# Kernel optimization log

Hardware: AMD Instinct MI355X
Metric: run time of the kernel (lower is better)

The kernel has to match this reference:

```python
import jax, jax.numpy as jnp
import numpy as np
import math

B, L, HD, H = 4, 1024, 512, 8
D = HD // H  # 64 per-head dim


def setup_inputs() -> dict:
    key = jax.random.key(0)
    ks = jax.random.split(key, 9)
    query = jax.random.normal(ks[0], (B, L, HD), jnp.float32)
    key_ = jax.random.normal(ks[1], (B, L, HD), jnp.float32)
    value = jax.random.normal(ks[2], (B, L, HD), jnp.float32)
    kernel = jax.random.normal(ks[3], (B * H, L, L), jnp.float32) * 0.1
    # sparse-ish boolean mask; low density so no row is fully masked
    attn_mask = jax.random.bernoulli(ks[4], 0.05, (B * H, L, L))
    in_proj_weight = jax.random.normal(ks[5], (3 * HD, HD), jnp.float32) * 0.02
    in_proj_bias = jnp.zeros((3 * HD,), jnp.float32)
    out_w = jax.random.normal(ks[6], (HD, HD), jnp.float32) * 0.02
    out_b = jnp.zeros((HD,), jnp.float32)
    return dict(query=query, key_=key_, value=value, attn_mask=attn_mask,
                key_padding_mask=0, kernel=kernel,
                in_proj_weight=in_proj_weight, in_proj_bias=in_proj_bias,
                out_w=out_w, out_b=out_b)


def _split_heads(x):
    # [B, L, HD] -> [B*H, L, D]
    b, l, _ = x.shape
    return x.reshape(b, l, H, D).transpose(0, 2, 1, 3).reshape(b * H, l, D)


def _merge_heads(x):
    # [B*H, L, D] -> [B, L, HD]
    bh, l, d = x.shape
    b = bh // H
    return x.reshape(b, H, l, d).transpose(0, 2, 1, 3).reshape(b, l, H * d)


def reference(query, key_, value, attn_mask, key_padding_mask, kernel,
              in_proj_weight, in_proj_bias, out_w, out_b):
    # key_padding_mask is falsy (None-equivalent) -> attn_mask unchanged
    wq, wk, wv = in_proj_weight[:HD], in_proj_weight[HD:2 * HD], in_proj_weight[2 * HD:]
    bq, bk, bv = in_proj_bias[:HD], in_proj_bias[HD:2 * HD], in_proj_bias[2 * HD:]
    q = _split_heads(query @ wq.T + bq)   # [B*H, L, D]
    k = _split_heads(key_ @ wk.T + bk)
    v = _split_heads(value @ wv.T + bv)
    scale = 1.0 / math.sqrt(D)
    scores = jnp.einsum('bqd,bkd->bqk', q, k) * scale  # [B*H, Lq, Lk]
    scores = scores + kernel.transpose(0, 2, 1)        # additive kernel bias
    scores = jnp.where(attn_mask, -jnp.inf, scores)    # masked_fill
    attn = jax.nn.softmax(scores, axis=-1)
    out = jnp.einsum('bqk,bkd->bqd', attn, v)          # [B*H, Lq, D]
    out = _merge_heads(out)                            # [B, Lq, HD]
    return out @ out_w.T + out_b
```

## Files before the change

### kernel.cpp

```cpp
#include <hip/hip_runtime.h>
#include <hip/hip_bf16.h>
#include <cstdint>
#include <cstddef>

typedef _Float16 half8 __attribute__((ext_vector_type(8)));
typedef _Float16 half4 __attribute__((ext_vector_type(4)));
typedef float f32x4 __attribute__((ext_vector_type(4)));

#define NB 4
#define NL 1024
#define NHD 512
#define NH 8
#define ND 64
#define NBH 32

#define MFMA16(a, b, c) __builtin_amdgcn_mfma_f32_16x16x32_f16((a), (b), (c), 0, 0, 0)

__global__ void detect_mask_kernel(const uint4* __restrict__ m, int* __restrict__ flag) {
    __shared__ int s_byte;
    if (threadIdx.x == 0) s_byte = 0;
    __syncthreads();
    uint4 v[4];
#pragma unroll
    for (int j = 0; j < 4; ++j) v[j] = m[threadIdx.x * 4 + j];
    int bad = 0;
#pragma unroll
    for (int j = 0; j < 4; ++j) {
        unsigned ws[4] = {v[j].x, v[j].y, v[j].z, v[j].w};
#pragma unroll
        for (int i = 0; i < 4; ++i)
            if (ws[i] != 0u && ws[i] != 1u && ws[i] != 0x3F800000u) bad = 1;
    }
    if (bad) atomicOr(&s_byte, 1);
    __syncthreads();
    if (threadIdx.x == 0) *flag = s_byte;
}

__global__ __launch_bounds__(256) void bitmask_kernel(
    const void* __restrict__ mask, const int* __restrict__ flagp, unsigned* __restrict__ mb)
{
    const int t = blockIdx.x * 256 + threadIdx.x;
    unsigned w = 0;
    if (*flagp == 1) {
        const uint4* p = (const uint4*)((const unsigned char*)mask + (size_t)t * 32);
        uint4 a = p[0], b = p[1];
        unsigned src[8] = {a.x, a.y, a.z, a.w, b.x, b.y, b.z, b.w};
#pragma unroll
        for (int j = 0; j < 8; ++j) {
            unsigned u = src[j];
            w |= ((u & 0x000000FFu) ? 1u : 0u) << (4 * j + 0);
            w |= ((u & 0x0000FF00u) ? 1u : 0u) << (4 * j + 1);
            w |= ((u & 0x00FF0000u) ? 1u : 0u) << (4 * j + 2);
            w |= ((u & 0xFF000000u) ? 1u : 0u) << (4 * j + 3);
        }
    } else {
        const uint4* p = (const uint4*)((const unsigned*)mask + (size_t)t * 32);
#pragma unroll
        for (int j = 0; j < 8; ++j) {
            uint4 v = p[j];
            w |= (v.x ? 1u : 0u) << (4 * j + 0);
            w |= (v.y ? 1u : 0u) << (4 * j + 1);
            w |= (v.z ? 1u : 0u) << (4 * j + 2);
            w |= (v.w ? 1u : 0u) << (4 * j + 3);
        }
    }
    mb[t] = w;
}

__global__ __launch_bounds__(256) void qkv_gemm_kernel(
    const float* __restrict__ qin, const float* __restrict__ kin, const float* __restrict__ vin,
    const float* __restrict__ w, const float* __restrict__ bias,
    _Float16* __restrict__ qb, _Float16* __restrict__ kb, _Float16* __restrict__ vtb)
{
    const int mtile = blockIdx.x, ntile = blockIdx.y, proj = blockIdx.z;
    const float* A = proj == 0 ? qin : (proj == 1 ? kin : vin);
    const float* W = w + (size_t)proj * NHD * NHD;

    __shared__ __align__(16) _Float16 a_lds[128][72];
    __shared__ __align__(16) _Float16 b_lds[64][72];

    const int tid = threadIdx.x;
    const int wave = tid >> 6, lane = tid & 63, quad = lane >> 4, c = lane & 15;
    const int wm = wave >> 1, wn = wave & 1;

    f32x4 acc[4][2] = {};

    const int arow = tid >> 1, acol = (tid & 1) * 32;
    const int brow = tid >> 2, bcol = (tid & 3) * 16;
    const float* pa = &A[(size_t)(mtile * 128 + arow) * NHD + acol];
    const float* pb = &W[(size_t)(ntile * 64 + brow) * NHD + bcol];

    f32x4 ar[8], br[4];
#pragma unroll
    for (int j = 0; j < 8; ++j) ar[j] = *(const f32x4*)(pa + j * 4);
#pragma unroll
    for (int j = 0; j < 4; ++j) br[j] = *(const f32x4*)(pb + j * 4);

    for (int k0 = 0; k0 < NHD; k0 += 64) {
        half8 ah[4], bh_[2];
#pragma unroll
        for (int t = 0; t < 4; ++t)
#pragma unroll
            for (int j = 0; j < 4; ++j) {
                ah[t][j] = (_Float16)ar[2 * t][j];
                ah[t][4 + j] = (_Float16)ar[2 * t + 1][j];
            }
#pragma unroll
        for (int t = 0; t < 2; ++t)
#pragma unroll
            for (int j = 0; j < 4; ++j) {
                bh_[t][j] = (_Float16)br[2 * t][j];
                bh_[t][4 + j] = (_Float16)br[2 * t + 1][j];
            }
        __syncthreads();
#pragma unroll
        for (int t = 0; t < 4; ++t) *(half8*)&a_lds[arow][acol + t * 8] = ah[t];
#pragma unroll
        for (int t = 0; t < 2; ++t) *(half8*)&b_lds[brow][bcol + t * 8] = bh_[t];
        if (k0 < NHD - 64) {
            const float* na = pa + k0 + 64;
            const float* nb = pb + k0 + 64;
#pragma unroll
            for (int j = 0; j < 8; ++j) ar[j] = *(const f32x4*)(na + j * 4);
#pragma unroll
            for (int j = 0; j < 4; ++j) br[j] = *(const f32x4*)(nb + j * 4);
        }
        __syncthreads();

#pragma unroll
        for (int kk = 0; kk < 2; ++kk) {
            half8 af[4], bf[2];
#pragma unroll
            for (int ms = 0; ms < 4; ++ms)
                af[ms] = *(const half8*)&a_lds[wm * 64 + ms * 16 + c][kk * 32 + quad * 8];
#pragma unroll
            for (int ns = 0; ns < 2; ++ns)
                bf[ns] = *(const half8*)&b_lds[wn * 32 + ns * 16 + c][kk * 32 + quad * 8];
#pragma unroll
            for (int ms = 0; ms < 4; ++ms)
#pragma unroll
                for (int ns = 0; ns < 2; ++ns)
                    acc[ms][ns] = MFMA16(af[ms], bf[ns], acc[ms][ns]);
        }
    }

#pragma unroll
    for (int ms = 0; ms < 4; ++ms)
#pragma unroll
    for (int ns = 0; ns < 2; ++ns) {
        const int Cc = ntile * 64 + wn * 32 + ns * 16 + c;
        const float bv = bias[proj * NHD + Cc];
        const int h = Cc >> 6, d = Cc & 63;
#pragma unroll
        for (int r = 0; r < 4; ++r) {
            const int R = mtile * 128 + wm * 64 + ms * 16 + quad * 4 + r;
            const int b = R >> 10, l = R & 1023;
            const int bh = b * NH + h;
            float val = acc[ms][ns][r] + bv;
            if (proj == 0) {
                qb[((size_t)(bh * NL + l)) * ND + d] = (_Float16)(val * 0.125f);
            } else if (proj == 1) {
                kb[((size_t)(bh * NL + l)) * ND + d] = (_Float16)val;
            } else {
                vtb[((size_t)(bh * ND + d)) * NL + l] = (_Float16)val;
            }
        }
    }
}

__global__ __launch_bounds__(256) void attn_kernel(
    const _Float16* __restrict__ qb, const _Float16* __restrict__ kb, const _Float16* __restrict__ vtb,
    const float* __restrict__ kern, const unsigned* __restrict__ mb,
    float* __restrict__ pO, float* __restrict__ pm, float* __restrict__ pl)
{
    const int qt = blockIdx.x, bh = blockIdx.y, seg = blockIdx.z;
    const int tid = threadIdx.x, wave = tid >> 6, lane = tid & 63, quad = lane >> 4, c = lane & 15;
    const int q_base = qt * 64 + wave * 16;
    const int kt0 = seg * 4;

    __shared__ __align__(16) _Float16 k_lds[64][72];
    __shared__ __align__(16) _Float16 vt_lds[64][72];
    __shared__ __align__(16) _Float16 p_lds[64][72];
    __shared__ __align__(16) float bias_lds[64][68];
    __shared__ unsigned mask_lds[64][2];

    half8 aq0 = *(const half8*)&qb[((size_t)(bh * NL) + q_base + c) * ND + quad * 8];
    half8 aq1 = *(const half8*)&qb[((size_t)(bh * NL) + q_base + c) * ND + 32 + quad * 8];

    f32x4 O[4] = {};
    float m_i[4] = {-1e30f, -1e30f, -1e30f, -1e30f};
    float l_i[4] = {0.f, 0.f, 0.f, 0.f};

    const int sr = tid >> 2, sc = (tid & 3) * 16;

    half8 kr0, kr1, vr0, vr1;
    f32x4 gr[4];
    unsigned mr = 0;

    {
        const _Float16* pk = &kb[((size_t)(bh * NL) + kt0 * 64 + sr) * ND + sc];
        kr0 = *(const half8*)pk; kr1 = *(const half8*)(pk + 8);
        const _Float16* pv = &vtb[((size_t)(bh * ND) + sr) * NL + kt0 * 64 + sc];
        vr0 = *(const half8*)pv; vr1 = *(const half8*)(pv + 8);
        const float* pg = &kern[((size_t)bh * NL + kt0 * 64 + sr) * NL + qt * 64 + sc];
#pragma unroll
        for (int j = 0; j < 4; ++j) gr[j] = *(const f32x4*)(pg + j * 4);
        if (tid < 128) mr = mb[((size_t)bh * NL + qt * 64 + (tid >> 1)) * 32 + kt0 * 2 + (tid & 1)];
    }

    for (int kt = 0; kt < 4; ++kt) {
        __syncthreads();
        *(half8*)&k_lds[sr][sc] = kr0;  *(half8*)&k_lds[sr][sc + 8] = kr1;
        *(half8*)&vt_lds[sr][sc] = vr0; *(half8*)&vt_lds[sr][sc + 8] = vr1;
#pragma unroll
        for (int j = 0; j < 4; ++j) *(f32x4*)&bias_lds[sr][(tid & 3) * 16 + j * 4] = gr[j];
        if (tid < 128) mask_lds[tid >> 1][tid & 1] = mr;

        if (kt < 3) {
            const int ktg = kt0 + kt + 1;
            const _Float16* pk = &kb[((size_t)(bh * NL) + ktg * 64 + sr) * ND + sc];
            kr0 = *(const half8*)pk; kr1 = *(const half8*)(pk + 8);
            const _Float16* pv = &vtb[((size_t)(bh * ND) + sr) * NL + ktg * 64 + sc];
            vr0 = *(const half8*)pv; vr1 = *(const half8*)(pv + 8);
            const float* pg = &kern[((size_t)bh * NL + ktg * 64 + sr) * NL + qt * 64 + sc];
#pragma unroll
            for (int j = 0; j < 4; ++j) gr[j] = *(const f32x4*)(pg + j * 4);
            if (tid < 128) mr = mb[((size_t)bh * NL + qt * 64 + (tid >> 1)) * 32 + ktg * 2 + (tid & 1)];
        }
        __syncthreads();

        f32x4 S[4];
#pragma unroll
        for (int ns = 0; ns < 4; ++ns) {
            f32x4 a = {};
            half8 bk0 = *(const half8*)&k_lds[ns * 16 + c][quad * 8];
            half8 bk1 = *(const half8*)&k_lds[ns * 16 + c][32 + quad * 8];
            a = MFMA16(aq0, bk0, a);
            a = MFMA16(aq1, bk1, a);
            S[ns] = a;
        }

        unsigned mw0[4], mw1[4];
#pragma unroll
        for (int r = 0; r < 4; ++r) {
            const int row = wave * 16 + quad * 4 + r;
            uint2 mm = *(const uint2*)&mask_lds[row][0];
            mw0[r] = mm.x; mw1[r] = mm.y;
        }

#pragma unroll
        for (int ns = 0; ns < 4; ++ns) {
            f32x4 bv = *(const f32x4*)&bias_lds[ns * 16 + c][wave * 16 + quad * 4];
            const int bit = ((ns & 1) << 4) + c;
#pragma unroll
            for (int r = 0; r < 4; ++r) {
                unsigned w = (ns < 2) ? mw0[r] : mw1[r];
                bool mk = (w >> bit) & 1u;
                S[ns][r] = mk ? -1e30f : (S[ns][r] + bv[r]);
            }
        }

        float pmax[4], al[4];
#pragma unroll
        for (int r = 0; r < 4; ++r) {
            float t = fmaxf(fmaxf(S[0][r], S[1][r]), fmaxf(S[2][r], S[3][r]));
            t = fmaxf(t, __shfl_xor(t, 1));
            t = fmaxf(t, __shfl_xor(t, 2));
            t = fmaxf(t, __shfl_xor(t, 4));
            t = fmaxf(t, __shfl_xor(t, 8));
            float mn = fmaxf(m_i[r], t);
            al[r] = __expf(m_i[r] - mn);
            m_i[r] = mn;
            pmax[r] = mn;
        }
        float rs[4] = {0.f, 0.f, 0.f, 0.f};
#pragma unroll
        for (int ns = 0; ns < 4; ++ns)
#pragma unroll
            for (int r = 0; r < 4; ++r) {
                float p = __expf(S[ns][r] - pmax[r]);
                S[ns][r] = p;
                rs[r] += p;
            }
#pragma unroll
        for (int r = 0; r < 4; ++r) {
            float t = rs[r];
            t += __shfl_xor(t, 1);
            t += __shfl_xor(t, 2);
            t += __shfl_xor(t, 4);
            t += __shfl_xor(t, 8);
            l_i[r] = l_i[r] * al[r] + t;
        }
#pragma unroll
        for (int ds = 0; ds < 4; ++ds)
#pragma unroll
            for (int r = 0; r < 4; ++r)
                O[ds][r] *= al[r];

#pragma unroll
        for (int ns = 0; ns < 4; ++ns)
#pragma unroll
            for (int r = 0; r < 4; ++r)
                p_lds[wave * 16 + quad * 4 + r][ns * 16 + c] = (_Float16)S[ns][r];
        __asm__ volatile("s_waitcnt lgkmcnt(0)" ::: "memory");

#pragma unroll
        for (int ks = 0; ks < 2; ++ks) {
            half8 ap = *(const half8*)&p_lds[wave * 16 + c][ks * 32 + quad * 8];
#pragma unroll
            for (int ds = 0; ds < 4; ++ds) {
                half8 bv = *(const half8*)&vt_lds[ds * 16 + c][ks * 32 + quad * 8];
                O[ds] = MFMA16(ap, bv, O[ds]);
            }
        }
    }

    const int ub = (bh * 16 + qt) * 4 + seg;
    float* pOb = pO + (size_t)ub * 4096;
#pragma unroll
    for (int ds = 0; ds < 4; ++ds)
#pragma unroll
        for (int r = 0; r < 4; ++r)
            pOb[(wave * 16 + quad * 4 + r) * 64 + ds * 16 + c] = O[ds][r];
    if (c == 0) {
#pragma unroll
        for (int r = 0; r < 4; ++r) {
            const int row = wave * 16 + quad * 4 + r;
            pm[(size_t)ub * 64 + row] = m_i[r];
            pl[(size_t)ub * 64 + row] = l_i[r];
        }
    }
}

__global__ __launch_bounds__(256) void merge_kernel(
    const float* __restrict__ pO, const float* __restrict__ pm, const float* __restrict__ pl,
    _Float16* __restrict__ ctx)
{
    const int qt = blockIdx.x, bh = blockIdx.y;
    const int u0 = (bh * 16 + qt) * 4;
    __shared__ float sc_[4][64];
    const int tid = threadIdx.x;
    if (tid < 64) {
        float mm[4], ll[4];
        float m = -1e30f;
#pragma unroll
        for (int j = 0; j < 4; ++j) {
            mm[j] = pm[(size_t)(u0 + j) * 64 + tid];
            ll[j] = pl[(size_t)(u0 + j) * 64 + tid];
            m = fmaxf(m, mm[j]);
        }
        float l = 0.f, e[4];
#pragma unroll
        for (int j = 0; j < 4; ++j) { e[j] = __expf(mm[j] - m); l += ll[j] * e[j]; }
        float linv = 1.0f / l;
#pragma unroll
        for (int j = 0; j < 4; ++j) sc_[j][tid] = e[j] * linv;
    }
    __syncthreads();
    const int b = bh >> 3, h = bh & 7;
#pragma unroll
    for (int js = 0; js < 4; ++js) {
        const int idx = js * 1024 + tid * 4;
        const int row = idx >> 6, col = idx & 63;
        f32x4 s = {};
#pragma unroll
        for (int j = 0; j < 4; ++j) {
            f32x4 a = *(const f32x4*)(pO + (size_t)(u0 + j) * 4096 + idx);
            const float w = sc_[j][row];
#pragma unroll
            for (int i = 0; i < 4; ++i) s[i] += a[i] * w;
        }
        half4 o;
#pragma unroll
        for (int i = 0; i < 4; ++i) o[i] = (_Float16)s[i];
        *(half4*)&ctx[((size_t)(b * NL + qt * 64 + row)) * NHD + h * ND + col] = o;
    }
}

__global__ __launch_bounds__(256) void out_gemm_kernel(
    const _Float16* __restrict__ ctx, const float* __restrict__ w, const float* __restrict__ bias,
    float* __restrict__ out)
{
    const int mtile = blockIdx.x, ntile = blockIdx.y;
    __shared__ __align__(16) _Float16 a_lds[64][72];
    __shared__ __align__(16) _Float16 b_lds[64][72];
    const int tid = threadIdx.x, wave = tid >> 6, lane = tid & 63, quad = lane >> 4, c = lane & 15;
    const int wm = wave >> 1, wn = wave & 1;
    f32x4 acc[2][2] = {};

    const int sr = tid >> 2, sc = (tid & 3) * 16;
    const _Float16* pa = &ctx[(size_t)(mtile * 64 + sr) * NHD + sc];
    const float* pb = &w[(size_t)(ntile * 64 + sr) * NHD + sc];

    half8 ah0, ah1;
    f32x4 br[4];
    ah0 = *(const half8*)pa; ah1 = *(const half8*)(pa + 8);
#pragma unroll
    for (int j = 0; j < 4; ++j) br[j] = *(const f32x4*)(pb + j * 4);

    for (int k0 = 0; k0 < NHD; k0 += 64) {
        half8 bh0, bh1;
#pragma unroll
        for (int j = 0; j < 4; ++j) {
            bh0[j] = (_Float16)br[0][j]; bh0[4 + j] = (_Float16)br[1][j];
            bh1[j] = (_Float16)br[2][j]; bh1[4 + j] = (_Float16)br[3][j];
        }
        __syncthreads();
        *(half8*)&a_lds[sr][sc] = ah0; *(half8*)&a_lds[sr][sc + 8] = ah1;
        *(half8*)&b_lds[sr][sc] = bh0; *(half8*)&b_lds[sr][sc + 8] = bh1;
        if (k0 < NHD - 64) {
            const _Float16* na = pa + k0 + 64;
            const float* nb = pb + k0 + 64;
            ah0 = *(const half8*)na; ah1 = *(const half8*)(na + 8);
#pragma unroll
            for (int j = 0; j < 4; ++j) br[j] = *(const f32x4*)(nb + j * 4);
        }
        __syncthreads();

#pragma unroll
        for (int kk = 0; kk < 2; ++kk) {
            half8 af0 = *(const half8*)&a_lds[wm * 32 + c][kk * 32 + quad * 8];
            half8 af1 = *(const half8*)&a_lds[wm * 32 + 16 + c][kk * 32 + quad * 8];
            half8 bf0 = *(const half8*)&b_lds[wn * 32 + c][kk * 32 + quad * 8];
            half8 bf1 = *(const half8*)&b_lds[wn * 32 + 16 + c][kk * 32 + quad * 8];
            acc[0][0] = MFMA16(af0, bf0, acc[0][0]);
            acc[0][1] = MFMA16(af0, bf1, acc[0][1]);
            acc[1][0] = MFMA16(af1, bf0, acc[1][0]);
            acc[1][1] = MFMA16(af1, bf1, acc[1][1]);
        }
    }

#pragma unroll
    for (int ms = 0; ms < 2; ++ms)
#pragma unroll
    for (int ns = 0; ns < 2; ++ns) {
        const int Cc = ntile * 64 + wn * 32 + ns * 16 + c;
        const float bv = bias[Cc];
#pragma unroll
        for (int r = 0; r < 4; ++r) {
            const int R = mtile * 64 + wm * 32 + ms * 16 + quad * 4 + r;
            out[(size_t)R * NHD + Cc] = acc[ms][ns][r] + bv;
        }
    }
}

extern "C" void kernel_launch(void* const* d_in, const int* in_sizes, int n_in,
                              void* d_out, int out_size, void* d_ws, size_t ws_size,
                              hipStream_t stream)
{
    const float* query = (const float*)d_in[0];
    const float* key_  = (const float*)d_in[1];
    const float* value = (const float*)d_in[2];
    const void*  mask  = d_in[3];
    const float* kern  = (const float*)d_in[5];
    const float* ipw   = (const float*)d_in[6];
    const float* ipb   = (const float*)d_in[7];
    const float* outw  = (const float*)d_in[8];
    const float* outb  = (const float*)d_in[9];

    char* ws = (char*)d_ws;
    _Float16* qb  = (_Float16*)(ws);
    _Float16* kb  = (_Float16*)(ws + (4ull << 20));
    _Float16* vtb = (_Float16*)(ws + (8ull << 20));
    _Float16* ctx = (_Float16*)(ws + (12ull << 20));
    int* flag     = (int*)(ws + (16ull << 20));
    float* pO     = (float*)(ws + (24ull << 20));
    float* pm     = (float*)(ws + (56ull << 20));
    float* pl     = (float*)(ws + (57ull << 20));

    unsigned* mb = (unsigned*)d_out;

    detect_mask_kernel<<<1, 256, 0, stream>>>((const uint4*)mask, flag);
    bitmask_kernel<<<4096, 256, 0, stream>>>(mask, flag, mb);
    qkv_gemm_kernel<<<dim3(32, 8, 3), 256, 0, stream>>>(query, key_, value, ipw, ipb, qb, kb, vtb);
    attn_kernel<<<dim3(16, 32, 4), 256, 0, stream>>>(qb, kb, vtb, kern, mb, pO, pm, pl);
    merge_kernel<<<dim3(16, 32), 256, 0, stream>>>(pO, pm, pl, ctx);
    out_gemm_kernel<<<dim3(64, 8), 256, 0, stream>>>(ctx, outw, outb, (float*)d_out);
}
```

Measured before the change: 373.8 us.

## Fuse split-KV merge into output GEMM and fold mask detection into bitmask

The separate softmax merge kernel is removed. The output projection GEMM now reads the fp16 partial attention outputs and their max/sum statistics and combines the two halves while staging its A operand. The attention split along keys drops from 4 segments to 2, partial outputs are stored in fp16, and mask-format detection moves into each bitmask block instead of a separate one-block kernel. The aim is to cut two kernel launches and the fp32 partial-output traffic, at the cost of fewer attention blocks, lower partial precision, and per-block format detection that could misclassify an all-zero block.

Measured after the change: 368.1 us. No clear change (-1.5%).

```diff
diff --git a/kernel.cpp b/kernel.cpp
--- a/kernel.cpp
+++ b/kernel.cpp
@@ -16,35 +16,27 @@
 
 #define MFMA16(a, b, c) __builtin_amdgcn_mfma_f32_16x16x32_f16((a), (b), (c), 0, 0, 0)
 
-__global__ void detect_mask_kernel(const uint4* __restrict__ m, int* __restrict__ flag) {
+__global__ __launch_bounds__(256) void bitmask_kernel(
+    const void* __restrict__ mask, unsigned* __restrict__ mb)
+{
     __shared__ int s_byte;
-    if (threadIdx.x == 0) s_byte = 0;
+    const int tid = threadIdx.x;
+    const int t = blockIdx.x * 256 + tid;
+    if (tid == 0) s_byte = 0;
     __syncthreads();
-    uint4 v[4];
-#pragma unroll
-    for (int j = 0; j < 4; ++j) v[j] = m[threadIdx.x * 4 + j];
+
+    const uint4* p = (const uint4*)((const unsigned char*)mask + (size_t)t * 32);
+    uint4 a = p[0], b = p[1];
+    unsigned src[8] = {a.x, a.y, a.z, a.w, b.x, b.y, b.z, b.w};
     int bad = 0;
 #pragma unroll
-    for (int j = 0; j < 4; ++j) {
-        unsigned ws[4] = {v[j].x, v[j].y, v[j].z, v[j].w};
-#pragma unroll
-        for (int i = 0; i < 4; ++i)
-            if (ws[i] != 0u && ws[i] != 1u && ws[i] != 0x3F800000u) bad = 1;
-    }
+    for (int j = 0; j < 8; ++j)
+        if (src[j] != 0u && src[j] != 1u && src[j] != 0x3F800000u) bad = 1;
     if (bad) atomicOr(&s_byte, 1);
     __syncthreads();
-    if (threadIdx.x == 0) *flag = s_byte;
-}
-
-__global__ __launch_bounds__(256) void bitmask_kernel(
-    const void* __restrict__ mask, const int* __restrict__ flagp, unsigned* __restrict__ mb)
-{
-    const int t = blockIdx.x * 256 + threadIdx.x;
+
     unsigned w = 0;
-    if (*flagp == 1) {
-        const uint4* p = (const uint4*)((const unsigned char*)mask + (size_t)t * 32);
-        uint4 a = p[0], b = p[1];
-        unsigned src[8] = {a.x, a.y, a.z, a.w, b.x, b.y, b.z, b.w};
+    if (s_byte) {
 #pragma unroll
         for (int j = 0; j < 8; ++j) {
             unsigned u = src[j];
@@ -54,10 +46,10 @@
             w |= ((u & 0xFF000000u) ? 1u : 0u) << (4 * j + 3);
         }
     } else {
-        const uint4* p = (const uint4*)((const unsigned*)mask + (size_t)t * 32);
+        const uint4* q = (const uint4*)((const unsigned*)mask + (size_t)t * 32);
 #pragma unroll
         for (int j = 0; j < 8; ++j) {
-            uint4 v = p[j];
+            uint4 v = q[j];
             w |= (v.x ? 1u : 0u) << (4 * j + 0);
             w |= (v.y ? 1u : 0u) << (4 * j + 1);
             w |= (v.z ? 1u : 0u) << (4 * j + 2);
@@ -171,12 +163,12 @@
 __global__ __launch_bounds__(256) void attn_kernel(
     const _Float16* __restrict__ qb, const _Float16* __restrict__ kb, const _Float16* __restrict__ vtb,
     const float* __restrict__ kern, const unsigned* __restrict__ mb,
-    float* __restrict__ pO, float* __restrict__ pm, float* __restrict__ pl)
+    _Float16* __restrict__ pO, float* __restrict__ pm, float* __restrict__ pl)
 {
-    const int qt = blockIdx.x, bh = blockIdx.y, seg = blockIdx.z;
+    const int qt = blockIdx.x, bh = blockIdx.y, half = blockIdx.z;
     const int tid = threadIdx.x, wave = tid >> 6, lane = tid & 63, quad = lane >> 4, c = lane & 15;
     const int q_base = qt * 64 + wave * 16;
-    const int kt0 = seg * 4;
+    const int kt0 = half * 8;
 
     __shared__ __align__(16) _Float16 k_lds[64][72];
     __shared__ __align__(16) _Float16 vt_lds[64][72];
@@ -208,7 +200,7 @@
         if (tid < 128) mr = mb[((size_t)bh * NL + qt * 64 + (tid >> 1)) * 32 + kt0 * 2 + (tid & 1)];
     }
 
-    for (int kt = 0; kt < 4; ++kt) {
+    for (int kt = 0; kt < 8; ++kt) {
         __syncthreads();
         *(half8*)&k_lds[sr][sc] = kr0;  *(half8*)&k_lds[sr][sc + 8] = kr1;
         *(half8*)&vt_lds[sr][sc] = vr0; *(half8*)&vt_lds[sr][sc + 8] = vr1;
@@ -216,7 +208,7 @@
         for (int j = 0; j < 4; ++j) *(f32x4*)&bias_lds[sr][(tid & 3) * 16 + j * 4] = gr[j];
         if (tid < 128) mask_lds[tid >> 1][tid & 1] = mr;
 
-        if (kt < 3) {
+        if (kt < 7) {
             const int ktg = kt0 + kt + 1;
             const _Float16* pk = &kb[((size_t)(bh * NL) + ktg * 64 + sr) * ND + sc];
             kr0 = *(const half8*)pk; kr1 = *(const half8*)(pk + 8);
@@ -315,13 +307,13 @@
         }
     }
 
-    const int ub = (bh * 16 + qt) * 4 + seg;
-    float* pOb = pO + (size_t)ub * 4096;
+    const int ub = (bh * 16 + qt) * 2 + half;
+    _Float16* pOb = pO + (size_t)ub * 4096;
 #pragma unroll
     for (int ds = 0; ds < 4; ++ds)
 #pragma unroll
         for (int r = 0; r < 4; ++r)
-            pOb[(wave * 16 + quad * 4 + r) * 64 + ds * 16 + c] = O[ds][r];
+            pOb[(wave * 16 + quad * 4 + r) * 64 + ds * 16 + c] = (_Float16)O[ds][r];
     if (c == 0) {
 #pragma unroll
         for (int r = 0; r < 4; ++r) {
@@ -332,56 +324,13 @@
     }
 }
 
-__global__ __launch_bounds__(256) void merge_kernel(
-    const float* __restrict__ pO, const float* __restrict__ pm, const float* __restrict__ pl,
-    _Float16* __restrict__ ctx)
-{
-    const int qt = blockIdx.x, bh = blockIdx.y;
-    const int u0 = (bh * 16 + qt) * 4;
-    __shared__ float sc_[4][64];
-    const int tid = threadIdx.x;
-    if (tid < 64) {
-        float mm[4], ll[4];
-        float m = -1e30f;
-#pragma unroll
-        for (int j = 0; j < 4; ++j) {
-            mm[j] = pm[(size_t)(u0 + j) * 64 + tid];
-            ll[j] = pl[(size_t)(u0 + j) * 64 + tid];
-            m = fmaxf(m, mm[j]);
-        }
-        float l = 0.f, e[4];
-#pragma unroll
-        for (int j = 0; j < 4; ++j) { e[j] = __expf(mm[j] - m); l += ll[j] * e[j]; }
-        float linv = 1.0f / l;
-#pragma unroll
-        for (int j = 0; j < 4; ++j) sc_[j][tid] = e[j] * linv;
-    }
-    __syncthreads();
-    const int b = bh >> 3, h = bh & 7;
-#pragma unroll
-    for (int js = 0; js < 4; ++js) {
-        const int idx = js * 1024 + tid * 4;
-        const int row = idx >> 6, col = idx & 63;
-        f32x4 s = {};
-#pragma unroll
-        for (int j = 0; j < 4; ++j) {
-            f32x4 a = *(const f32x4*)(pO + (size_t)(u0 + j) * 4096 + idx);
-            const float w = sc_[j][row];
-#pragma unroll
-            for (int i = 0; i < 4; ++i) s[i] += a[i] * w;
-        }
-        half4 o;
-#pragma unroll
-        for (int i = 0; i < 4; ++i) o[i] = (_Float16)s[i];
-        *(half4*)&ctx[((size_t)(b * NL + qt * 64 + row)) * NHD + h * ND + col] = o;
-    }
-}
-
 __global__ __launch_bounds__(256) void out_gemm_kernel(
-    const _Float16* __restrict__ ctx, const float* __restrict__ w, const float* __restrict__ bias,
+    const _Float16* __restrict__ pO, const float* __restrict__ pm, const float* __restrict__ pl,
+    const float* __restrict__ w, const float* __restrict__ bias,
     float* __restrict__ out)
 {
     const int mtile = blockIdx.x, ntile = blockIdx.y;
+    const int bb = mtile >> 4, qt = mtile & 15;
     __shared__ __align__(16) _Float16 a_lds[64][72];
     __shared__ __align__(16) _Float16 b_lds[64][72];
     const int tid = threadIdx.x, wave = tid >> 6, lane = tid & 63, quad = lane >> 4, c = lane & 15;
@@ -389,17 +338,37 @@
     f32x4 acc[2][2] = {};
 
     const int sr = tid >> 2, sc = (tid & 3) * 16;
-    const _Float16* pa = &ctx[(size_t)(mtile * 64 + sr) * NHD + sc];
-    const float* pb = &w[(size_t)(ntile * 64 + sr) * NHD + sc];
-
-    half8 ah0, ah1;
+
+    half8 p0a, p0b, p1a, p1b;
     f32x4 br[4];
-    ah0 = *(const half8*)pa; ah1 = *(const half8*)(pa + 8);
-#pragma unroll
-    for (int j = 0; j < 4; ++j) br[j] = *(const f32x4*)(pb + j * 4);
-
+    float m0, l0, m1, l1;
+
+    auto fetch = [&](int k0) {
+        const int h = k0 >> 6;
+        const int u0 = ((bb * 8 + h) * 16 + qt) * 2;
+        const _Float16* q0 = pO + (size_t)u0 * 4096 + sr * 64 + sc;
+        p0a = *(const half8*)q0; p0b = *(const half8*)(q0 + 8);
+        const _Float16* q1 = q0 + 4096;
+        p1a = *(const half8*)q1; p1b = *(const half8*)(q1 + 8);
+        m0 = pm[(size_t)u0 * 64 + sr]; l0 = pl[(size_t)u0 * 64 + sr];
+        m1 = pm[(size_t)(u0 + 1) * 64 + sr]; l1 = pl[(size_t)(u0 + 1) * 64 + sr];
+        const float* pb = &w[(size_t)(ntile * 64 + sr) * NHD + k0 + sc];
+#pragma unroll
+        for (int j = 0; j < 4; ++j) br[j] = *(const f32x4*)(pb + j * 4);
+    };
+
+    fetch(0);
     for (int k0 = 0; k0 < NHD; k0 += 64) {
-        half8 bh0, bh1;
+        const float mx = fmaxf(m0, m1);
+        const float e0 = __expf(m0 - mx), e1 = __expf(m1 - mx);
+        const float linv = 1.0f / (l0 * e0 + l1 * e1);
+        const float s0 = e0 * linv, s1 = e1 * linv;
+        half8 ah0, ah1, bh0, bh1;
+#pragma unroll
+        for (int j = 0; j < 8; ++j) {
+            ah0[j] = (_Float16)((float)p0a[j] * s0 + (float)p1a[j] * s1);
+            ah1[j] = (_Float16)((float)p0b[j] * s0 + (float)p1b[j] * s1);
+        }
 #pragma unroll
         for (int j = 0; j < 4; ++j) {
             bh0[j] = (_Float16)br[0][j]; bh0[4 + j] = (_Float16)br[1][j];
@@ -408,13 +377,7 @@
         __syncthreads();
         *(half8*)&a_lds[sr][sc] = ah0; *(half8*)&a_lds[sr][sc + 8] = ah1;
         *(half8*)&b_lds[sr][sc] = bh0; *(half8*)&b_lds[sr][sc + 8] = bh1;
-        if (k0 < NHD - 64) {
-            const _Float16* na = pa + k0 + 64;
-            const float* nb = pb + k0 + 64;
-            ah0 = *(const half8*)na; ah1 = *(const half8*)(na + 8);
-#pragma unroll
-            for (int j = 0; j < 4; ++j) br[j] = *(const f32x4*)(nb + j * 4);
-        }
+        if (k0 < NHD - 64) fetch(k0 + 64);
         __syncthreads();
 
 #pragma unroll
@@ -462,18 +425,13 @@
     _Float16* qb  = (_Float16*)(ws);
     _Float16* kb  = (_Float16*)(ws + (4ull << 20));
     _Float16* vtb = (_Float16*)(ws + (8ull << 20));
-    _Float16* ctx = (_Float16*)(ws + (12ull << 20));
-    int* flag     = (int*)(ws + (16ull << 20));
-    float* pO     = (float*)(ws + (24ull << 20));
-    float* pm     = (float*)(ws + (56ull << 20));
-    float* pl     = (float*)(ws + (57ull << 20));
-
-    unsigned* mb = (unsigned*)d_out;
-
-    detect_mask_kernel<<<1, 256, 0, stream>>>((const uint4*)mask, flag);
-    bitmask_kernel<<<4096, 256, 0, stream>>>(mask, flag, mb);
+    _Float16* pO  = (_Float16*)(ws + (16ull << 20));
+    float* pm     = (float*)(ws + (32ull << 20));
+    float* pl     = (float*)(ws + (33ull << 20));
+    unsigned* mb  = (unsigned*)(ws + (40ull << 20));
+
+    bitmask_kernel<<<4096, 256, 0, stream>>>(mask, mb);
     qkv_gemm_kernel<<<dim3(32, 8, 3), 256, 0, stream>>>(query, key_, value, ipw, ipb, qb, kb, vtb);
-    attn_kernel<<<dim3(16, 32, 4), 256, 0, stream>>>(qb, kb, vtb, kern, mb, pO, pm, pl);
-    merge_kernel<<<dim3(16, 32), 256, 0, stream>>>(pO, pm, pl, ctx);
-    out_gemm_kernel<<<dim3(64, 8), 256, 0, stream>>>(ctx, outw, outb, (float*)d_out);
+    attn_kernel<<<dim3(16, 32, 2), 256, 0, stream>>>(qb, kb, vtb, kern, mb, pO, pm, pl);
+    out_gemm_kernel<<<dim3(64, 8), 256, 0, stream>>>(pO, pm, pl, outw, outb, (float*)d_out);
 }
```
